# Kernel optimization log

Hardware: AMD Instinct MI355X
Metric: run time of the kernel (lower is better)

## Reference

```python
import jax, jax.numpy as jnp
import numpy as np

B, D, M, C = 1024, 64, 3, 16384

def setup_inputs() -> dict:
    key = jax.random.key(0)
    ks = jax.random.split(key, 8)
    # unit-norm features (as in contrastive learning) keep exp() in range
    f = jax.random.normal(ks[0], (B, D), jnp.float32)
    f_I = jax.random.normal(ks[1], (B, D), jnp.float32)
    f = f / jnp.linalg.norm(f, axis=1, keepdims=True)
    f_I = f_I / jnp.linalg.norm(f_I, axis=1, keepdims=True)
    cen = jax.random.normal(ks[2], (M, C, D), jnp.float32)
    cen_I = jax.random.normal(ks[3], (M, C, D), jnp.float32)
    cen = cen / jnp.linalg.norm(cen, axis=2, keepdims=True)
    cen_I = cen_I / jnp.linalg.norm(cen_I, axis=2, keepdims=True)
    # concentrations in [0.5, 1.5): positive temperatures
    conc = jax.random.uniform(ks[4], (M, C), jnp.float32) + 0.5
    conc_I = jax.random.uniform(ks[5], (M, C), jnp.float32) + 0.5
    lab = jax.random.randint(ks[6], (M, B), 0, C, jnp.int64 if jax.config.jax_enable_x64 else jnp.int32)
    lab_I = jax.random.randint(ks[7], (M, B), 0, C, jnp.int64 if jax.config.jax_enable_x64 else jnp.int32)
    return {"features": f, "features_I": f_I, "M_kmeans": cen, "M_kmeans_I": cen_I,
            "concentrations": conc, "concentrations_I": conc_I,
            "labels": lab, "labels_I": lab_I, "lb": 1}

def _branch_loss(centroids, feats, conc, labels):
    # centroids: [M,C,D], feats: [B,D], conc: [M,C], labels: [M,B]
    # logits[m,c,b] = (centroids[m,c] . feats[b]) / conc[m,c]
    logits = jnp.einsum('mcd,bd->mcb', centroids, feats) / conc[:, :, None]
    exp_logits = jnp.exp(logits)                       # [M,C,B]
    log_sum = jnp.sum(exp_logits, axis=1)              # [M,B]
    pos = jnp.take_along_axis(exp_logits, labels[:, None, :], axis=1)[:, 0, :]  # [M,B]
    return jnp.sum(jnp.log(pos / log_sum))             # scalar (summed over m and b)

def reference(features, features_I, M_kmeans, M_kmeans_I,
              concentrations, concentrations_I, labels, labels_I, lb):
    m_num = M_kmeans.shape[0]
    batch_size = features.shape[0]
    t = _branch_loss(M_kmeans, features_I, concentrations, labels)
    t_I = _branch_loss(M_kmeans_I, features, concentrations_I, labels_I)
    return (1.0 / batch_size) * lb * (-1.0 / m_num) * 0.5 * (t + t_I)
```

## Files before the change

kernel.cpp:

```cpp
#include <hip/hip_runtime.h>

#define B_  1024
#define D_  64
#define M_  3
#define C_  16384

typedef __attribute__((ext_vector_type(8))) short bf16x8;
typedef __attribute__((ext_vector_type(4))) float f32x4;

__device__ __forceinline__ unsigned bfpack2(float lo, float hi) {
    return __builtin_amdgcn_perm(__float_as_uint(hi), __float_as_uint(lo),
                                 0x07060302u);
}
__device__ __forceinline__ bf16x8 pack8(float4 x, float4 y) {
    union { unsigned u[4]; bf16x8 v; } r;
    r.u[0] = bfpack2(x.x, x.y);
    r.u[1] = bfpack2(x.z, x.w);
    r.u[2] = bfpack2(y.x, y.y);
    r.u[3] = bfpack2(y.z, y.w);
    return r.v;
}
__device__ __forceinline__ float fexp2(float x) {
    float r; asm("v_exp_f32 %0, %1" : "=v"(r) : "v"(x)); return r;
}


__global__ __launch_bounds__(256) void prep(
    const float* __restrict__ f, const float* __restrict__ f_I,
    unsigned short* __restrict__ fb0, unsigned short* __restrict__ fb1,
    float* __restrict__ wz)
{
    const int t = blockIdx.x * 256 + threadIdx.x;
    const float4 a = reinterpret_cast<const float4*>(f_I)[t];
    const float4 b = reinterpret_cast<const float4*>(f)[t];
    uint2 pa, pb;
    pa.x = bfpack2(a.x, a.y); pa.y = bfpack2(a.z, a.w);
    pb.x = bfpack2(b.x, b.y); pb.y = bfpack2(b.z, b.w);
    reinterpret_cast<uint2*>(fb0)[t] = pa;
    reinterpret_cast<uint2*>(fb1)[t] = pb;
    if (t < 6272) wz[t] = 0.0f;
}

__global__ __launch_bounds__(256) void lse_mfma(
    const float* __restrict__ cen0, const float* __restrict__ cen1,
    const unsigned short* __restrict__ fb0, const unsigned short* __restrict__ fb1,
    const float* __restrict__ conc0, const float* __restrict__ conc1,
    float* __restrict__ wsum)
{
    const int br = blockIdx.z;
    const int m  = blockIdx.y;
    const float* __restrict__ cen  = br ? cen1  : cen0;
    const float* __restrict__ conc = br ? conc1 : conc0;
    const unsigned short* __restrict__ fb = br ? fb1 : fb0;

    __shared__ float lsum[B_];
    for (int i = threadIdx.x; i < B_; i += 256) lsum[i] = 0.0f;
    __syncthreads();

    const int wave = threadIdx.x >> 6;
    const int lane = threadIdx.x & 63;
    const int lrow = lane & 15;
    const int lk   = lane >> 4;
    const float LOG2E = 1.44269504088896340736f;

    bf16x8 af[2][2];
#pragma unroll
    for (int t = 0; t < 2; ++t) {
        const int row = blockIdx.x * 128 + wave * 32 + t * 16 + lrow;
        const float sc = LOG2E * __builtin_amdgcn_rcpf(conc[m * C_ + row]);
        const float* cp = cen + (size_t)(m * C_ + row) * D_ + lk * 8;
        float4 x0 = *reinterpret_cast<const float4*>(cp);
        float4 x1 = *reinterpret_cast<const float4*>(cp + 4);
        float4 y0 = *reinterpret_cast<const float4*>(cp + 32);
        float4 y1 = *reinterpret_cast<const float4*>(cp + 36);
        x0.x *= sc; x0.y *= sc; x0.z *= sc; x0.w *= sc;
        x1.x *= sc; x1.y *= sc; x1.z *= sc; x1.w *= sc;
        y0.x *= sc; y0.y *= sc; y0.z *= sc; y0.w *= sc;
        y1.x *= sc; y1.y *= sc; y1.z *= sc; y1.w *= sc;
        af[t][0] = pack8(x0, x1);
        af[t][1] = pack8(y0, y1);
    }

    const unsigned short* fp = fb + lrow * D_ + lk * 8;
    bf16x8 nb0 = *reinterpret_cast<const bf16x8*>(fp);
    bf16x8 nb1 = *reinterpret_cast<const bf16x8*>(fp + 32);

    for (int bt = 0; bt < B_ / 16; ++bt) {
        const bf16x8 b0 = nb0, b1 = nb1;
        if (bt + 1 < B_ / 16) {
            const unsigned short* np = fp + (size_t)(bt + 1) * 16 * D_;
            nb0 = *reinterpret_cast<const bf16x8*>(np);
            nb1 = *reinterpret_cast<const bf16x8*>(np + 32);
        }
        f32x4 acc0 = {0.f, 0.f, 0.f, 0.f};
        f32x4 acc1 = {0.f, 0.f, 0.f, 0.f};
        acc0 = __builtin_amdgcn_mfma_f32_16x16x32_bf16(af[0][0], b0, acc0, 0, 0, 0);
        acc0 = __builtin_amdgcn_mfma_f32_16x16x32_bf16(af[0][1], b1, acc0, 0, 0, 0);
        acc1 = __builtin_amdgcn_mfma_f32_16x16x32_bf16(af[1][0], b0, acc1, 0, 0, 0);
        acc1 = __builtin_amdgcn_mfma_f32_16x16x32_bf16(af[1][1], b1, acc1, 0, 0, 0);

        const float e0 = fexp2(acc0[0]), e1 = fexp2(acc0[1]);
        const float e2 = fexp2(acc0[2]), e3 = fexp2(acc0[3]);
        const float e4 = fexp2(acc1[0]), e5 = fexp2(acc1[1]);
        const float e6 = fexp2(acc1[2]), e7 = fexp2(acc1[3]);
        float s = ((e0 + e1) + (e2 + e3)) + ((e4 + e5) + (e6 + e7));

        s += __shfl_xor(s, 16);
        s += __shfl_xor(s, 32);
        if (lane < 16) atomicAdd(&lsum[bt * 16 + lane], s);
    }

    __syncthreads();
    float* __restrict__ wdst = wsum + (br * M_ + m) * B_;
    for (int i = threadIdx.x; i < B_; i += 256)
        atomicAdd(&wdst[i], lsum[i]);
}

__global__ __launch_bounds__(256) void finish(
    const float* __restrict__ f,    const float* __restrict__ f_I,
    const float* __restrict__ cen0, const float* __restrict__ cen1,
    const float* __restrict__ conc0,const float* __restrict__ conc1,
    const int*   __restrict__ lab0, const int*   __restrict__ lab1,
    const float* __restrict__ wsum, float* __restrict__ wsred)
{
    const int idx = blockIdx.x * 256 + threadIdx.x;
    const int br  = idx / (M_ * B_);
    const int r   = idx - br * (M_ * B_);
    const int m   = r / B_;
    const int b   = r - m * B_;

    const float* cen  = br ? cen1  : cen0;
    const float* conc = br ? conc1 : conc0;
    const int*   lab  = br ? lab1  : lab0;
    const float* ft   = br ? f     : f_I;

    const int c = lab[r];
    const float* cr   = cen + (size_t)(m * C_ + c) * D_;
    const float* frow = ft + (size_t)b * D_;
    float a0 = 0.f, a1 = 0.f, a2 = 0.f, a3 = 0.f;
#pragma unroll
    for (int d = 0; d < D_; d += 4) {
        a0 = fmaf(cr[d + 0], frow[d + 0], a0);
        a1 = fmaf(cr[d + 1], frow[d + 1], a1);
        a2 = fmaf(cr[d + 2], frow[d + 2], a2);
        a3 = fmaf(cr[d + 3], frow[d + 3], a3);
    }
    const float logit = ((a0 + a1) + (a2 + a3)) / conc[(size_t)m * C_ + c];
    float term = logit - __logf(wsum[idx]);

#pragma unroll
    for (int off = 32; off > 0; off >>= 1)
        term += __shfl_down(term, off);
    if ((threadIdx.x & 63) == 0)
        wsred[idx >> 6] = term;
}

__global__ void finalize(const float* __restrict__ wsred,
                         const int*   __restrict__ lb,
                         float* __restrict__ out)
{
    const int t = threadIdx.x;
    float v = wsred[t];
    if (t < 32) v += wsred[64 + t];
#pragma unroll
    for (int off = 32; off > 0; off >>= 1)
        v += __shfl_down(v, off);
    if (t == 0)
        out[0] = (1.0f / (float)B_) * (float)lb[0] * (-1.0f / (float)M_)
                 * 0.5f * v;
}

extern "C" void kernel_launch(void* const* d_in, const int* in_sizes, int n_in,
                              void* d_out, int out_size, void* d_ws, size_t ws_size,
                              hipStream_t stream) {
    const float* f      = (const float*)d_in[0];
    const float* f_I    = (const float*)d_in[1];
    const float* cen    = (const float*)d_in[2];
    const float* cen_I  = (const float*)d_in[3];
    const float* conc   = (const float*)d_in[4];
    const float* conc_I = (const float*)d_in[5];
    const int*   lab    = (const int*)d_in[6];
    const int*   lab_I  = (const int*)d_in[7];
    const int*   lb     = (const int*)d_in[8];

    float* ws    = (float*)d_ws;
    float* wsum  = ws;
    float* wsred = ws + 6144;
    unsigned short* fb0 = (unsigned short*)(ws + 6400);
    unsigned short* fb1 = fb0 + B_ * D_;
    float* out = (float*)d_out;

    prep<<<64, 256, 0, stream>>>(f, f_I, fb0, fb1, wsum);

    dim3 g(C_ / 128, M_, 2);
    lse_mfma<<<g, 256, 0, stream>>>(cen, cen_I, fb0, fb1, conc, conc_I, wsum);

    finish<<<(2 * M_ * B_) / 256, 256, 0, stream>>>(
        f, f_I, cen, cen_I, conc, conc_I, lab, lab_I, wsum, wsred);

    finalize<<<1, 64, 0, stream>>>(wsred, lb, out);
}
```

Before: 143.8 us.

## Swap operand roles: keep features in registers, stream centroids with XCD-aware mapping

The logsumexp kernel now holds a 64-row slice of features as the resident MFMA operand and streams 16-row centroid tiles through each wave. Centroids are converted to bf16 on the fly, and the per-centroid temperature is applied after the MFMA. Partial sums stay in registers across the C loop and are reduced with shuffles, replacing per-iteration LDS atomics and removing the separate bf16 prep pass. Block IDs are remapped so all blocks on one XCD share a centroid chunk for L2 locality. The cost is more redundant centroid reads, since each centroid is fetched once per feature block (16x), plus more fp32 to bf16 pack work per iteration.

Result: slower. 150.4 us (+4.6%).

```diff
diff --git a/kernel.cpp b/kernel.cpp
--- a/kernel.cpp
+++ b/kernel.cpp
@@ -25,95 +25,126 @@
 }
 
 
-__global__ __launch_bounds__(256) void prep(
-    const float* __restrict__ f, const float* __restrict__ f_I,
-    unsigned short* __restrict__ fb0, unsigned short* __restrict__ fb1,
-    float* __restrict__ wz)
-{
-    const int t = blockIdx.x * 256 + threadIdx.x;
-    const float4 a = reinterpret_cast<const float4*>(f_I)[t];
-    const float4 b = reinterpret_cast<const float4*>(f)[t];
-    uint2 pa, pb;
-    pa.x = bfpack2(a.x, a.y); pa.y = bfpack2(a.z, a.w);
-    pb.x = bfpack2(b.x, b.y); pb.y = bfpack2(b.z, b.w);
-    reinterpret_cast<uint2*>(fb0)[t] = pa;
-    reinterpret_cast<uint2*>(fb1)[t] = pb;
-    if (t < 6272) wz[t] = 0.0f;
-}
-
-__global__ __launch_bounds__(256) void lse_mfma(
+__global__ __launch_bounds__(256) void zero_ws(float* __restrict__ ws) {
+    int i = blockIdx.x * 256 + threadIdx.x;
+    if (i < 6272) ws[i] = 0.0f;
+}
+
+__global__ __launch_bounds__(256, 4) void lse_mfma(
     const float* __restrict__ cen0, const float* __restrict__ cen1,
-    const unsigned short* __restrict__ fb0, const unsigned short* __restrict__ fb1,
-    const float* __restrict__ conc0, const float* __restrict__ conc1,
+    const float* __restrict__ f0,   const float* __restrict__ f1,
+    const float* __restrict__ conc0,const float* __restrict__ conc1,
     float* __restrict__ wsum)
 {
-    const int br = blockIdx.z;
-    const int m  = blockIdx.y;
+    const int bid  = blockIdx.x;
+    const int xcd  = bid & 7;
+    const int idx  = bid >> 3;
+    const int pair = idx >> 4;
+    const int bblk = idx & 15;
+    const int pid  = xcd * 12 + pair;
+    const int cchunk = pid & 15;
+    const int mbr    = pid >> 4;
+    const int br = mbr & 1, m = mbr >> 1;
+
     const float* __restrict__ cen  = br ? cen1  : cen0;
+    const float* __restrict__ ft   = br ? f1    : f0;
     const float* __restrict__ conc = br ? conc1 : conc0;
-    const unsigned short* __restrict__ fb = br ? fb1 : fb0;
-
-    __shared__ float lsum[B_];
-    for (int i = threadIdx.x; i < B_; i += 256) lsum[i] = 0.0f;
-    __syncthreads();
-
-    const int wave = threadIdx.x >> 6;
+
+    const int wv   = threadIdx.x >> 6;
     const int lane = threadIdx.x & 63;
     const int lrow = lane & 15;
     const int lk   = lane >> 4;
+    const int wbase = bblk * 64;
     const float LOG2E = 1.44269504088896340736f;
 
-    bf16x8 af[2][2];
-#pragma unroll
-    for (int t = 0; t < 2; ++t) {
-        const int row = blockIdx.x * 128 + wave * 32 + t * 16 + lrow;
-        const float sc = LOG2E * __builtin_amdgcn_rcpf(conc[m * C_ + row]);
-        const float* cp = cen + (size_t)(m * C_ + row) * D_ + lk * 8;
-        float4 x0 = *reinterpret_cast<const float4*>(cp);
-        float4 x1 = *reinterpret_cast<const float4*>(cp + 4);
-        float4 y0 = *reinterpret_cast<const float4*>(cp + 32);
-        float4 y1 = *reinterpret_cast<const float4*>(cp + 36);
-        x0.x *= sc; x0.y *= sc; x0.z *= sc; x0.w *= sc;
-        x1.x *= sc; x1.y *= sc; x1.z *= sc; x1.w *= sc;
-        y0.x *= sc; y0.y *= sc; y0.z *= sc; y0.w *= sc;
-        y1.x *= sc; y1.y *= sc; y1.z *= sc; y1.w *= sc;
+    bf16x8 af[4][2];
+#pragma unroll
+    for (int t = 0; t < 4; ++t) {
+        const float* fp = ft + (size_t)(wbase + t * 16 + lrow) * D_ + lk * 8;
+        float4 x0 = *reinterpret_cast<const float4*>(fp);
+        float4 x1 = *reinterpret_cast<const float4*>(fp + 4);
+        float4 y0 = *reinterpret_cast<const float4*>(fp + 32);
+        float4 y1 = *reinterpret_cast<const float4*>(fp + 36);
         af[t][0] = pack8(x0, x1);
         af[t][1] = pack8(y0, y1);
     }
 
-    const unsigned short* fp = fb + lrow * D_ + lk * 8;
-    bf16x8 nb0 = *reinterpret_cast<const bf16x8*>(fp);
-    bf16x8 nb1 = *reinterpret_cast<const bf16x8*>(fp + 32);
-
-    for (int bt = 0; bt < B_ / 16; ++bt) {
-        const bf16x8 b0 = nb0, b1 = nb1;
-        if (bt + 1 < B_ / 16) {
-            const unsigned short* np = fp + (size_t)(bt + 1) * 16 * D_;
-            nb0 = *reinterpret_cast<const bf16x8*>(np);
-            nb1 = *reinterpret_cast<const bf16x8*>(np + 32);
+    const int cb = cchunk * 1024 + wv * 256;
+    const float* bp = cen  + (size_t)(m * C_ + cb + lrow) * D_ + lk * 8;
+    const float* cp = conc + m * C_ + cb + lrow;
+
+    float4 n0 = *reinterpret_cast<const float4*>(bp);
+    float4 n1 = *reinterpret_cast<const float4*>(bp + 4);
+    float4 n2 = *reinterpret_cast<const float4*>(bp + 32);
+    float4 n3 = *reinterpret_cast<const float4*>(bp + 36);
+    float  nc = *cp;
+
+    float s[4][4];
+#pragma unroll
+    for (int t = 0; t < 4; ++t)
+#pragma unroll
+        for (int j = 0; j < 4; ++j) s[t][j] = 0.0f;
+
+    for (int ct = 0; ct < 16; ++ct) {
+        const float4 c0 = n0, c1 = n1, c2 = n2, c3 = n3;
+        const float  cc = nc;
+        if (ct + 1 < 16) {
+            bp += 16 * D_; cp += 16;
+            n0 = *reinterpret_cast<const float4*>(bp);
+            n1 = *reinterpret_cast<const float4*>(bp + 4);
+            n2 = *reinterpret_cast<const float4*>(bp + 32);
+            n3 = *reinterpret_cast<const float4*>(bp + 36);
+            nc = *cp;
         }
-        f32x4 acc0 = {0.f, 0.f, 0.f, 0.f};
-        f32x4 acc1 = {0.f, 0.f, 0.f, 0.f};
-        acc0 = __builtin_amdgcn_mfma_f32_16x16x32_bf16(af[0][0], b0, acc0, 0, 0, 0);
-        acc0 = __builtin_amdgcn_mfma_f32_16x16x32_bf16(af[0][1], b1, acc0, 0, 0, 0);
-        acc1 = __builtin_amdgcn_mfma_f32_16x16x32_bf16(af[1][0], b0, acc1, 0, 0, 0);
-        acc1 = __builtin_amdgcn_mfma_f32_16x16x32_bf16(af[1][1], b1, acc1, 0, 0, 0);
-
-        const float e0 = fexp2(acc0[0]), e1 = fexp2(acc0[1]);
-        const float e2 = fexp2(acc0[2]), e3 = fexp2(acc0[3]);
-        const float e4 = fexp2(acc1[0]), e5 = fexp2(acc1[1]);
-        const float e6 = fexp2(acc1[2]), e7 = fexp2(acc1[3]);
-        float s = ((e0 + e1) + (e2 + e3)) + ((e4 + e5) + (e6 + e7));
-
-        s += __shfl_xor(s, 16);
-        s += __shfl_xor(s, 32);
-        if (lane < 16) atomicAdd(&lsum[bt * 16 + lane], s);
-    }
-
+        const bf16x8 bk0 = pack8(c0, c1);
+        const bf16x8 bk1 = pack8(c2, c3);
+        const float  ic  = LOG2E * __builtin_amdgcn_rcpf(cc);
+
+        f32x4 a0 = {0.f,0.f,0.f,0.f}, a1 = {0.f,0.f,0.f,0.f};
+        f32x4 a2 = {0.f,0.f,0.f,0.f}, a3 = {0.f,0.f,0.f,0.f};
+        a0 = __builtin_amdgcn_mfma_f32_16x16x32_bf16(af[0][0], bk0, a0, 0, 0, 0);
+        a0 = __builtin_amdgcn_mfma_f32_16x16x32_bf16(af[0][1], bk1, a0, 0, 0, 0);
+        a1 = __builtin_amdgcn_mfma_f32_16x16x32_bf16(af[1][0], bk0, a1, 0, 0, 0);
+        a1 = __builtin_amdgcn_mfma_f32_16x16x32_bf16(af[1][1], bk1, a1, 0, 0, 0);
+        a2 = __builtin_amdgcn_mfma_f32_16x16x32_bf16(af[2][0], bk0, a2, 0, 0, 0);
+        a2 = __builtin_amdgcn_mfma_f32_16x16x32_bf16(af[2][1], bk1, a2, 0, 0, 0);
+        a3 = __builtin_amdgcn_mfma_f32_16x16x32_bf16(af[3][0], bk0, a3, 0, 0, 0);
+        a3 = __builtin_amdgcn_mfma_f32_16x16x32_bf16(af[3][1], bk1, a3, 0, 0, 0);
+
+#pragma unroll
+        for (int j = 0; j < 4; ++j) {
+            s[0][j] += fexp2(a0[j] * ic);
+            s[1][j] += fexp2(a1[j] * ic);
+            s[2][j] += fexp2(a2[j] * ic);
+            s[3][j] += fexp2(a3[j] * ic);
+        }
+    }
+
+    __shared__ float lsum[4][64];
+#pragma unroll
+    for (int t = 0; t < 4; ++t)
+#pragma unroll
+        for (int j = 0; j < 4; ++j) {
+            float v = s[t][j];
+            v += __shfl_xor(v, 1);
+            v += __shfl_xor(v, 2);
+            v += __shfl_xor(v, 4);
+            v += __shfl_xor(v, 8);
+            s[t][j] = v;
+        }
+    if (lrow == 0) {
+#pragma unroll
+        for (int t = 0; t < 4; ++t)
+#pragma unroll
+            for (int j = 0; j < 4; ++j)
+                lsum[wv][t * 16 + lk * 4 + j] = s[t][j];
+    }
     __syncthreads();
-    float* __restrict__ wdst = wsum + (br * M_ + m) * B_;
-    for (int i = threadIdx.x; i < B_; i += 256)
-        atomicAdd(&wdst[i], lsum[i]);
+    if (threadIdx.x < 64) {
+        const float v = lsum[0][threadIdx.x] + lsum[1][threadIdx.x]
+                      + lsum[2][threadIdx.x] + lsum[3][threadIdx.x];
+        atomicAdd(&wsum[(br * M_ + m) * B_ + wbase + threadIdx.x], v);
+    }
 }
 
 __global__ __launch_bounds__(256) void finish(
@@ -186,14 +217,11 @@
     float* ws    = (float*)d_ws;
     float* wsum  = ws;
     float* wsred = ws + 6144;
-    unsigned short* fb0 = (unsigned short*)(ws + 6400);
-    unsigned short* fb1 = fb0 + B_ * D_;
-    float* out = (float*)d_out;
-
-    prep<<<64, 256, 0, stream>>>(f, f_I, fb0, fb1, wsum);
-
-    dim3 g(C_ / 128, M_, 2);
-    lse_mfma<<<g, 256, 0, stream>>>(cen, cen_I, fb0, fb1, conc, conc_I, wsum);
+    float* out   = (float*)d_out;
+
+    zero_ws<<<25, 256, 0, stream>>>(ws);
+
+    lse_mfma<<<1536, 256, 0, stream>>>(cen, cen_I, f_I, f, conc, conc_I, wsum);
 
     finish<<<(2 * M_ * B_) / 256, 256, 0, stream>>>(
         f, f_I, cen, cen_I, conc, conc_I, lab, lab_I, wsum, wsred);
```
